# Performance work log

Measured on AMD Instinct MI355X. Metric: run time of the kernel, lower is better.

Reference implementation:

```python
import jax, jax.numpy as jnp
import numpy as np

NEG_SLOPE = 0.2
EPS = 1e-6


def _edge_type_conv(xs, xt, Ws, Wt, a, src, tgt):
    """One hetero edge type: GAT-like edge softmax (unnormalized exp / scatter-sum)."""
    sx = xs @ Ws              # [Ns, d]
    tx = xt @ Wt              # [Nt, d]
    d = sx.shape[1]
    sxg = sx[src]             # [E, d] gather source
    txg = tx[tgt]             # [E, d] gather target
    # concat([sxg, txg]) @ a  ==  sxg @ a[:d] + txg @ a[d:]  (avoids materializing concat)
    score = sxg @ a[:d] + txg @ a[d:]                 # [E, 1]
    att = jnp.exp(jax.nn.leaky_relu(score, NEG_SLOPE))  # [E, 1]
    Nt = xt.shape[0]
    msg = jax.ops.segment_sum(sxg * att, tgt, num_segments=Nt)  # [Nt, d]
    den = jax.ops.segment_sum(att, tgt, num_segments=Nt)        # [Nt, 1]
    return tx + msg / (den + EPS)


def setup_inputs() -> dict:
    key = jax.random.key(0)
    ks = jax.random.split(key, 10)
    N_USER, N_ITEM, D_IN, D_OUT, E = 100000, 100000, 128, 64, 1000000
    glorot_w = np.sqrt(6.0 / (D_IN + D_OUT))
    glorot_a = 1.414 * np.sqrt(6.0 / (2 * D_OUT + 1))
    return {
        "x_user": jax.random.normal(ks[0], (N_USER, D_IN), jnp.float32),
        "x_item": jax.random.normal(ks[1], (N_ITEM, D_IN), jnp.float32),
        "W_ui_src": jax.random.uniform(ks[2], (D_IN, D_OUT), jnp.float32, -glorot_w, glorot_w),
        "W_ui_tgt": jax.random.uniform(ks[3], (D_IN, D_OUT), jnp.float32, -glorot_w, glorot_w),
        "W_iu_src": jax.random.uniform(ks[4], (D_IN, D_OUT), jnp.float32, -glorot_w, glorot_w),
        "W_iu_tgt": jax.random.uniform(ks[5], (D_IN, D_OUT), jnp.float32, -glorot_w, glorot_w),
        "a_ui": jax.random.uniform(ks[6], (2 * D_OUT, 1), jnp.float32, -glorot_a, glorot_a),
        "a_iu": jax.random.uniform(ks[7], (2 * D_OUT, 1), jnp.float32, -glorot_a, glorot_a),
        "edge_ui": jax.random.randint(ks[8], (2, E), 0, N_USER),  # row0: user src, row1: item tgt
        "edge_iu": jax.random.randint(ks[9], (2, E), 0, N_ITEM),  # row0: item src, row1: user tgt
    }


def reference(x_user, x_item, W_ui_src, W_ui_tgt, W_iu_src, W_iu_tgt, a_ui, a_iu, edge_ui, edge_iu):
    # edge type (user, visits, item): target is item
    out_item = _edge_type_conv(x_user, x_item, W_ui_src, W_ui_tgt, a_ui, edge_ui[0], edge_ui[1])
    # edge type (item, visited_by, user): target is user
    out_user = _edge_type_conv(x_item, x_user, W_iu_src, W_iu_tgt, a_iu, edge_iu[0], edge_iu[1])
    return (out_user, out_item)
```

## Files before the change

### kernel.cpp

```cpp
#include <hip/hip_runtime.h>
#include <hip/hip_fp16.h>

#define NEG_SLOPE 0.2f
#define EPS 1e-6f
#define D_IN 128
#define D_OUT 64
#define BN2   192
#define CAP   2304
#define LHIST 2112
#define TILE  8192

__global__ __launch_bounds__(256) void gemm_score_dual(
    const float* __restrict__ x_user, const float* __restrict__ x_item,
    const float* __restrict__ W_ui_src, const float* __restrict__ W_ui_tgt,
    const float* __restrict__ W_iu_src, const float* __restrict__ W_iu_tgt,
    const float* __restrict__ a_ui, const float* __restrict__ a_iu,
    __half* __restrict__ sx_u, __half* __restrict__ sx_i,
    float* __restrict__ out_user, float* __restrict__ out_item,
    float* __restrict__ s_src_ui, float* __restrict__ t_tgt_iu,
    float* __restrict__ s_src_iu, float* __restrict__ t_tgt_ui,
    int nb_u, int N_USER, int N_ITEM)
{
    const bool is_item = (blockIdx.x >= (unsigned)nb_u);
    const float* X  = is_item ? x_item : x_user;
    const float* W1 = is_item ? W_iu_src : W_ui_src;
    const float* W2 = is_item ? W_ui_tgt : W_iu_tgt;
    const float* a1 = is_item ? a_iu : a_ui;
    const float* a2 = is_item ? (a_ui + 64) : (a_iu + 64);
    __half* sfeat   = is_item ? sx_i : sx_u;
    float* tout     = is_item ? out_item : out_user;
    float* s1       = is_item ? s_src_iu : s_src_ui;
    float* s2       = is_item ? t_tgt_ui : t_tgt_iu;
    const int N     = is_item ? N_ITEM : N_USER;
    const int br    = (is_item ? (blockIdx.x - nb_u) : blockIdx.x) * 64;

    __shared__ float Ws[32][128];
    __shared__ float Xs[64][36];
    const int tid = threadIdx.x;
    const int tx = tid & 15;
    const int ty = tid >> 4;

    float acc[4][8];
    #pragma unroll
    for (int r = 0; r < 4; ++r)
        #pragma unroll
        for (int c = 0; c < 8; ++c) acc[r][c] = 0.f;

    for (int kt = 0; kt < D_IN; kt += 32) {
        #pragma unroll
        for (int i = 0; i < 4; ++i) {
            int l = tid + i * 256;
            int row = l >> 5;
            int c4 = (l & 31) << 2;
            const float* wsrc = (c4 < 64) ? &W1[(kt + row) * 64 + c4]
                                          : &W2[(kt + row) * 64 + (c4 - 64)];
            *(float4*)&Ws[row][c4] = *(const float4*)wsrc;
        }
        #pragma unroll
        for (int i = 0; i < 2; ++i) {
            int l = tid + i * 256;
            int row = l >> 3;
            int c4 = (l & 7) << 2;
            float4 v = make_float4(0.f, 0.f, 0.f, 0.f);
            if (br + row < N)
                v = *(const float4*)&X[(size_t)(br + row) * D_IN + kt + c4];
            *(float4*)&Xs[row][c4] = v;
        }
        __syncthreads();
        #pragma unroll 4
        for (int k = 0; k < 32; ++k) {
            float4 wa = *(const float4*)&Ws[k][tx * 4];
            float4 wb = *(const float4*)&Ws[k][64 + tx * 4];
            #pragma unroll
            for (int r = 0; r < 4; ++r) {
                float xv = Xs[ty * 4 + r][k];
                acc[r][0] += xv * wa.x; acc[r][1] += xv * wa.y;
                acc[r][2] += xv * wa.z; acc[r][3] += xv * wa.w;
                acc[r][4] += xv * wb.x; acc[r][5] += xv * wb.y;
                acc[r][6] += xv * wb.z; acc[r][7] += xv * wb.w;
            }
        }
        __syncthreads();
    }

    float a1v[4], a2v[4];
    #pragma unroll
    for (int c = 0; c < 4; ++c) {
        a1v[c] = a1[tx * 4 + c];
        a2v[c] = a2[tx * 4 + c];
    }

    #pragma unroll
    for (int r = 0; r < 4; ++r) {
        int row = br + ty * 4 + r;
        float sv1 = acc[r][0] * a1v[0] + acc[r][1] * a1v[1]
                  + acc[r][2] * a1v[2] + acc[r][3] * a1v[3];
        float sv2 = acc[r][4] * a2v[0] + acc[r][5] * a2v[1]
                  + acc[r][6] * a2v[2] + acc[r][7] * a2v[3];
        sv1 += __shfl_xor(sv1, 1); sv2 += __shfl_xor(sv2, 1);
        sv1 += __shfl_xor(sv1, 2); sv2 += __shfl_xor(sv2, 2);
        sv1 += __shfl_xor(sv1, 4); sv2 += __shfl_xor(sv2, 4);
        sv1 += __shfl_xor(sv1, 8); sv2 += __shfl_xor(sv2, 8);
        if (row < N) {
            union { __half2 h[2]; uint2 u; } pk;
            pk.h[0] = __floats2half2_rn(acc[r][0], acc[r][1]);
            pk.h[1] = __floats2half2_rn(acc[r][2], acc[r][3]);
            *(uint2*)&sfeat[(size_t)row * 64 + tx * 4] = pk.u;
            *(float4*)&tout[(size_t)row * 64 + tx * 4] =
                make_float4(acc[r][4], acc[r][5], acc[r][6], acc[r][7]);
            if (tx == 0) { s1[row] = sv1; s2[row] = sv2; }
        }
    }
}

__global__ __launch_bounds__(512) void bucket_append(
    const int* __restrict__ edge_ui, const int* __restrict__ edge_iu,
    const float* __restrict__ s_src_ui, const float* __restrict__ t_tgt_ui,
    const float* __restrict__ s_src_iu, const float* __restrict__ t_tgt_iu,
    int* __restrict__ cnt, int2* __restrict__ payload,
    int E_a, int E_b, int NB_I, int NB)
{
    __shared__ int lhist[LHIST];
    __shared__ int lbase[LHIST];
    const int tid = threadIdx.x;
    const int ET = E_a + E_b;
    const int tstart = blockIdx.x * TILE;
    int tend = tstart + TILE; if (tend > ET) tend = ET;

    if (NB <= LHIST) {
        for (int i = tid; i < NB; i += 512) lhist[i] = 0;
        __syncthreads();
        for (int e = tstart + tid; e < tend; e += 512) {
            int b;
            if (e < E_a) b = edge_ui[E_a + e] / BN2;
            else         b = NB_I + edge_iu[E_b + (e - E_a)] / BN2;
            atomicAdd(&lhist[b], 1);
        }
        __syncthreads();
        for (int b = tid; b < NB; b += 512) {
            int c = lhist[b];
            lbase[b] = c ? atomicAdd(&cnt[b], c) : 0;
            lhist[b] = 0;
        }
        __syncthreads();
        for (int e = tstart + tid; e < tend; e += 512) {
            int s, t, b; float sc;
            if (e < E_a) {
                s = edge_ui[e]; t = edge_ui[E_a + e];
                sc = s_src_ui[s] + t_tgt_ui[t];
                b = t / BN2;
            } else {
                int eb = e - E_a;
                s = edge_iu[eb]; t = edge_iu[E_b + eb];
                sc = s_src_iu[s] + t_tgt_iu[t];
                b = NB_I + t / BN2;
            }
            sc = (sc > 0.f) ? sc : NEG_SLOPE * sc;
            float att = expf(sc);
            int tl = t % BN2;
            int pos = lbase[b] + atomicAdd(&lhist[b], 1);
            if (pos < CAP)
                payload[(size_t)b * CAP + pos] =
                    make_int2((tl << 20) | s, __float_as_int(att));
        }
    } else {
        for (int e = tstart + tid; e < tend; e += 512) {
            int s, t, b; float sc;
            if (e < E_a) {
                s = edge_ui[e]; t = edge_ui[E_a + e];
                sc = s_src_ui[s] + t_tgt_ui[t];
                b = t / BN2;
            } else {
                int eb = e - E_a;
                s = edge_iu[eb]; t = edge_iu[E_b + eb];
                sc = s_src_iu[s] + t_tgt_iu[t];
                b = NB_I + t / BN2;
            }
            sc = (sc > 0.f) ? sc : NEG_SLOPE * sc;
            float att = expf(sc);
            int tl = t % BN2;
            int pos = atomicAdd(&cnt[b], 1);
            if (pos < CAP)
                payload[(size_t)b * CAP + pos] =
                    make_int2((tl << 20) | s, __float_as_int(att));
        }
    }
}

__global__ __launch_bounds__(512) void bucket_reduce(
    const int* __restrict__ cnt, const int2* __restrict__ payload,
    const __half* __restrict__ sx_u, const __half* __restrict__ sx_i,
    float* __restrict__ out_user, float* __restrict__ out_item,
    int NB_I, int N_USER, int N_ITEM)
{
    __shared__ int2 ord[CAP];
    __shared__ int hist[BN2];
    __shared__ int sc[256];
    __shared__ int ofs[BN2];
    const int b = blockIdx.x;
    const bool item_side = (b < NB_I);
    const __half* sfeat = item_side ? sx_u : sx_i;
    float* outp = item_side ? out_item : out_user;
    const int tbase = (item_side ? b : b - NB_I) * BN2;
    const int Nside = item_side ? N_ITEM : N_USER;
    const int tid = threadIdx.x;

    int n = cnt[b]; if (n > CAP) n = CAP;
    const int2* pl = payload + (size_t)b * CAP;

    for (int i = tid; i < BN2; i += 512) hist[i] = 0;
    __syncthreads();
    for (int i = tid; i < n; i += 512) atomicAdd(&hist[pl[i].x >> 20], 1);
    __syncthreads();
    if (tid < 256) sc[tid] = (tid < BN2) ? hist[tid] : 0;
    __syncthreads();
    #pragma unroll
    for (int d = 1; d < 256; d <<= 1) {
        int v = 0;
        if (tid < 256 && tid >= d) v = sc[tid - d];
        __syncthreads();
        if (tid < 256) sc[tid] += v;
        __syncthreads();
    }
    if (tid < BN2) ofs[tid] = sc[tid] - hist[tid];
    __syncthreads();
    for (int i = tid; i < n; i += 512) {
        int2 p = pl[i];
        int pos = atomicAdd(&ofs[p.x >> 20], 1);
        ord[pos] = p;
    }
    __syncthreads();

    const int wave = tid >> 6, lane = tid & 63;
    for (int tl = wave; tl < BN2; tl += 8) {
        int en = sc[tl];
        int st = en - hist[tl];
        float msg0 = 0.f, msg1 = 0.f, msg2 = 0.f, msg3 = 0.f, den = 0.f;
        int j = st;
        for (; j + 3 < en; j += 4) {
            int2 pA = ord[j];
            int2 pB = ord[j + 1];
            int2 pC = ord[j + 2];
            int2 pD = ord[j + 3];
            float aA = __int_as_float(pA.y);
            float aB = __int_as_float(pB.y);
            float aC = __int_as_float(pC.y);
            float aD = __int_as_float(pD.y);
            float fA = __half2float(sfeat[(size_t)(pA.x & 0xFFFFF) * 64 + lane]);
            float fB = __half2float(sfeat[(size_t)(pB.x & 0xFFFFF) * 64 + lane]);
            float fC = __half2float(sfeat[(size_t)(pC.x & 0xFFFFF) * 64 + lane]);
            float fD = __half2float(sfeat[(size_t)(pD.x & 0xFFFFF) * 64 + lane]);
            msg0 += aA * fA;
            msg1 += aB * fB;
            msg2 += aC * fC;
            msg3 += aD * fD;
            den += (aA + aB) + (aC + aD);
        }
        for (; j < en; ++j) {
            int2 pA = ord[j];
            float aA = __int_as_float(pA.y);
            msg0 += aA * __half2float(sfeat[(size_t)(pA.x & 0xFFFFF) * 64 + lane]);
            den += aA;
        }
        int node = tbase + tl;
        if (node < Nside)
            outp[(size_t)node * 64 + lane] += ((msg0 + msg1) + (msg2 + msg3))
                                              / (den + EPS);
    }
}

extern "C" void kernel_launch(void* const* d_in, const int* in_sizes, int n_in,
                              void* d_out, int out_size, void* d_ws, size_t ws_size,
                              hipStream_t stream) {
    const float* x_user   = (const float*)d_in[0];
    const float* x_item   = (const float*)d_in[1];
    const float* W_ui_src = (const float*)d_in[2];
    const float* W_ui_tgt = (const float*)d_in[3];
    const float* W_iu_src = (const float*)d_in[4];
    const float* W_iu_tgt = (const float*)d_in[5];
    const float* a_ui     = (const float*)d_in[6];
    const float* a_iu     = (const float*)d_in[7];
    const int*   edge_ui  = (const int*)d_in[8];
    const int*   edge_iu  = (const int*)d_in[9];

    const int N_USER = in_sizes[0] / D_IN;
    const int N_ITEM = in_sizes[1] / D_IN;
    const int E_ui = in_sizes[8] / 2;
    const int E_iu = in_sizes[9] / 2;
    const int NMAX = (N_USER > N_ITEM) ? N_USER : N_ITEM;
    const int ET = E_ui + E_iu;
    const int NB_I = (N_ITEM + BN2 - 1) / BN2;
    const int NB_U = (N_USER + BN2 - 1) / BN2;
    const int NB = NB_I + NB_U;

    float* out = (float*)d_out;
    float* out_user = out;
    float* out_item = out + (size_t)N_USER * 64;

    float* w = (float*)d_ws;
    __half* sx_u = (__half*)w;  w += (size_t)NMAX * 32;
    __half* sx_i = (__half*)w;  w += (size_t)NMAX * 32;
    float* s_src_ui = w;  w += N_USER;
    float* t_tgt_iu = w;  w += N_USER;
    float* s_src_iu = w;  w += N_ITEM;
    float* t_tgt_ui = w;  w += N_ITEM;
    int* cnt = (int*)w;   w += (NB + 1) & ~1;
    int2* payload = (int2*)w;  w += (size_t)2 * NB * CAP;

    size_t need_bytes = (size_t)(w - (float*)d_ws) * sizeof(float);
    if (ws_size < need_bytes) return;

    int nb_u = (N_USER + 63) / 64;
    int nb_i = (N_ITEM + 63) / 64;

    gemm_score_dual<<<nb_u + nb_i, 256, 0, stream>>>(
        x_user, x_item, W_ui_src, W_ui_tgt, W_iu_src, W_iu_tgt, a_ui, a_iu,
        sx_u, sx_i, out_user, out_item,
        s_src_ui, t_tgt_iu, s_src_iu, t_tgt_ui,
        nb_u, N_USER, N_ITEM);

    hipMemsetAsync(cnt, 0, (size_t)NB * sizeof(int), stream);
    bucket_append<<<(ET + TILE - 1) / TILE, 512, 0, stream>>>(
        edge_ui, edge_iu, s_src_ui, t_tgt_ui, s_src_iu, t_tgt_iu,
        cnt, payload, E_ui, E_iu, NB_I, NB);

    bucket_reduce<<<NB, 512, 0, stream>>>(
        cnt, payload, sx_u, sx_i, out_user, out_item, NB_I, N_USER, N_ITEM);
}
```

Measured before the change: 385.3 us.

## Replace FP32 SIMT projection GEMM with fp16 MFMA and pre-transposed weights

```diff
diff --git a/kernel.cpp b/kernel.cpp
--- a/kernel.cpp
+++ b/kernel.cpp
@@ -10,10 +10,34 @@
 #define LHIST 2112
 #define TILE  8192
 
-__global__ __launch_bounds__(256) void gemm_score_dual(
-    const float* __restrict__ x_user, const float* __restrict__ x_item,
+typedef __attribute__((ext_vector_type(8))) _Float16 half8;
+typedef __attribute__((ext_vector_type(4))) float  floatx4;
+
+__global__ __launch_bounds__(256) void wt_transpose(
     const float* __restrict__ W_ui_src, const float* __restrict__ W_ui_tgt,
     const float* __restrict__ W_iu_src, const float* __restrict__ W_iu_tgt,
+    __half* __restrict__ wt_u, __half* __restrict__ wt_i)
+{
+    int t = blockIdx.x * 256 + threadIdx.x;
+    if (t >= 8192) return;
+    int kq = t & 31;
+    int c  = (t >> 5) & 127;
+    int side = t >> 12;
+    const float* W1 = side ? W_iu_src : W_ui_src;
+    const float* W2 = side ? W_ui_tgt : W_iu_tgt;
+    __half* wt = side ? wt_i : wt_u;
+    const float* W = (c < 64) ? W1 : W2;
+    int cc = c & 63;
+    __half h[4];
+    #pragma unroll
+    for (int j = 0; j < 4; ++j)
+        h[j] = __float2half(W[(kq * 4 + j) * 64 + cc]);
+    *(uint2*)&wt[(size_t)c * 128 + kq * 4] = *(uint2*)h;
+}
+
+__global__ __launch_bounds__(256) void gemm_mfma_dual(
+    const float* __restrict__ x_user, const float* __restrict__ x_item,
+    const __half* __restrict__ wt_u, const __half* __restrict__ wt_i,
     const float* __restrict__ a_ui, const float* __restrict__ a_iu,
     __half* __restrict__ sx_u, __half* __restrict__ sx_i,
     float* __restrict__ out_user, float* __restrict__ out_item,
@@ -22,94 +46,85 @@
     int nb_u, int N_USER, int N_ITEM)
 {
     const bool is_item = (blockIdx.x >= (unsigned)nb_u);
-    const float* X  = is_item ? x_item : x_user;
-    const float* W1 = is_item ? W_iu_src : W_ui_src;
-    const float* W2 = is_item ? W_ui_tgt : W_iu_tgt;
-    const float* a1 = is_item ? a_iu : a_ui;
-    const float* a2 = is_item ? (a_ui + 64) : (a_iu + 64);
-    __half* sfeat   = is_item ? sx_i : sx_u;
-    float* tout     = is_item ? out_item : out_user;
-    float* s1       = is_item ? s_src_iu : s_src_ui;
-    float* s2       = is_item ? t_tgt_ui : t_tgt_iu;
-    const int N     = is_item ? N_ITEM : N_USER;
-    const int br    = (is_item ? (blockIdx.x - nb_u) : blockIdx.x) * 64;
-
-    __shared__ float Ws[32][128];
-    __shared__ float Xs[64][36];
-    const int tid = threadIdx.x;
-    const int tx = tid & 15;
-    const int ty = tid >> 4;
-
-    float acc[4][8];
-    #pragma unroll
-    for (int r = 0; r < 4; ++r)
+    const float*  X    = is_item ? x_item : x_user;
+    const __half* Wt   = is_item ? wt_i : wt_u;
+    const float*  a1   = is_item ? a_iu : a_ui;
+    const float*  a2   = is_item ? (a_ui + 64) : (a_iu + 64);
+    __half* sfeat      = is_item ? sx_i : sx_u;
+    float*  tout       = is_item ? out_item : out_user;
+    float*  s1         = is_item ? s_src_iu : s_src_ui;
+    float*  s2         = is_item ? t_tgt_ui : t_tgt_iu;
+    const int N        = is_item ? N_ITEM : N_USER;
+    const int br       = (is_item ? (blockIdx.x - nb_u) : blockIdx.x) * 64;
+
+    const int lane = threadIdx.x & 63;
+    const int wv   = threadIdx.x >> 6;
+    const int m15  = lane & 15;
+    const int kg   = lane >> 4;
+    const int xrow = br + wv * 16 + m15;
+    const bool lvalid = (xrow < N);
+
+    floatx4 acc[8];
+    #pragma unroll
+    for (int t = 0; t < 8; ++t)
         #pragma unroll
-        for (int c = 0; c < 8; ++c) acc[r][c] = 0.f;
-
-    for (int kt = 0; kt < D_IN; kt += 32) {
+        for (int r = 0; r < 4; ++r) acc[t][r] = 0.f;
+
+    #pragma unroll
+    for (int kt = 0; kt < 4; ++kt) {
+        half8 afr = {};
+        if (lvalid) {
+            const float* xp = &X[(size_t)xrow * 128 + kt * 32 + kg * 8];
+            float4 x0 = *(const float4*)xp;
+            float4 x1 = *(const float4*)(xp + 4);
+            afr[0] = (_Float16)x0.x; afr[1] = (_Float16)x0.y;
+            afr[2] = (_Float16)x0.z; afr[3] = (_Float16)x0.w;
+            afr[4] = (_Float16)x1.x; afr[5] = (_Float16)x1.y;
+            afr[6] = (_Float16)x1.z; afr[7] = (_Float16)x1.w;
+        }
         #pragma unroll
-        for (int i = 0; i < 4; ++i) {
-            int l = tid + i * 256;
-            int row = l >> 5;
-            int c4 = (l & 31) << 2;
-            const float* wsrc = (c4 < 64) ? &W1[(kt + row) * 64 + c4]
-                                          : &W2[(kt + row) * 64 + (c4 - 64)];
-            *(float4*)&Ws[row][c4] = *(const float4*)wsrc;
-        }
+        for (int tn = 0; tn < 8; ++tn) {
+            half8 bfr = *(const half8*)&Wt[(size_t)(tn * 16 + m15) * 128
+                                           + kt * 32 + kg * 8];
+            acc[tn] = __builtin_amdgcn_mfma_f32_16x16x32_f16(afr, bfr,
+                                                             acc[tn], 0, 0, 0);
+        }
+    }
+
+    float av1[4], av2[4];
+    #pragma unroll
+    for (int tn = 0; tn < 4; ++tn) {
+        av1[tn] = a1[tn * 16 + m15];
+        av2[tn] = a2[tn * 16 + m15];
+    }
+    float sc1[4] = {0.f, 0.f, 0.f, 0.f}, sc2[4] = {0.f, 0.f, 0.f, 0.f};
+    const int srow0 = br + wv * 16 + kg * 4;
+    #pragma unroll
+    for (int tn = 0; tn < 8; ++tn) {
         #pragma unroll
-        for (int i = 0; i < 2; ++i) {
-            int l = tid + i * 256;
-            int row = l >> 3;
-            int c4 = (l & 7) << 2;
-            float4 v = make_float4(0.f, 0.f, 0.f, 0.f);
-            if (br + row < N)
-                v = *(const float4*)&X[(size_t)(br + row) * D_IN + kt + c4];
-            *(float4*)&Xs[row][c4] = v;
-        }
-        __syncthreads();
-        #pragma unroll 4
-        for (int k = 0; k < 32; ++k) {
-            float4 wa = *(const float4*)&Ws[k][tx * 4];
-            float4 wb = *(const float4*)&Ws[k][64 + tx * 4];
-            #pragma unroll
-            for (int r = 0; r < 4; ++r) {
-                float xv = Xs[ty * 4 + r][k];
-                acc[r][0] += xv * wa.x; acc[r][1] += xv * wa.y;
-                acc[r][2] += xv * wa.z; acc[r][3] += xv * wa.w;
-                acc[r][4] += xv * wb.x; acc[r][5] += xv * wb.y;
-                acc[r][6] += xv * wb.z; acc[r][7] += xv * wb.w;
+        for (int r = 0; r < 4; ++r) {
+            float v = acc[tn][r];
+            int srow = srow0 + r;
+            if (tn < 4) {
+                sc1[r] += v * av1[tn];
+                if (srow < N)
+                    sfeat[(size_t)srow * 64 + tn * 16 + m15] = __float2half(v);
+            } else {
+                sc2[r] += v * av2[tn - 4];
+                if (srow < N)
+                    tout[(size_t)srow * 64 + (tn - 4) * 16 + m15] = v;
             }
         }
-        __syncthreads();
-    }
-
-    float a1v[4], a2v[4];
-    #pragma unroll
-    for (int c = 0; c < 4; ++c) {
-        a1v[c] = a1[tx * 4 + c];
-        a2v[c] = a2[tx * 4 + c];
-    }
-
+    }
     #pragma unroll
     for (int r = 0; r < 4; ++r) {
-        int row = br + ty * 4 + r;
-        float sv1 = acc[r][0] * a1v[0] + acc[r][1] * a1v[1]
-                  + acc[r][2] * a1v[2] + acc[r][3] * a1v[3];
-        float sv2 = acc[r][4] * a2v[0] + acc[r][5] * a2v[1]
-                  + acc[r][6] * a2v[2] + acc[r][7] * a2v[3];
-        sv1 += __shfl_xor(sv1, 1); sv2 += __shfl_xor(sv2, 1);
-        sv1 += __shfl_xor(sv1, 2); sv2 += __shfl_xor(sv2, 2);
-        sv1 += __shfl_xor(sv1, 4); sv2 += __shfl_xor(sv2, 4);
-        sv1 += __shfl_xor(sv1, 8); sv2 += __shfl_xor(sv2, 8);
-        if (row < N) {
-            union { __half2 h[2]; uint2 u; } pk;
-            pk.h[0] = __floats2half2_rn(acc[r][0], acc[r][1]);
-            pk.h[1] = __floats2half2_rn(acc[r][2], acc[r][3]);
-            *(uint2*)&sfeat[(size_t)row * 64 + tx * 4] = pk.u;
-            *(float4*)&tout[(size_t)row * 64 + tx * 4] =
-                make_float4(acc[r][4], acc[r][5], acc[r][6], acc[r][7]);
-            if (tx == 0) { s1[row] = sv1; s2[row] = sv2; }
-        }
+        float v1 = sc1[r], v2 = sc2[r];
+        v1 += __shfl_xor(v1, 1); v2 += __shfl_xor(v2, 1);
+        v1 += __shfl_xor(v1, 2); v2 += __shfl_xor(v2, 2);
+        v1 += __shfl_xor(v1, 4); v2 += __shfl_xor(v2, 4);
+        v1 += __shfl_xor(v1, 8); v2 += __shfl_xor(v2, 8);
+        int srow = srow0 + r;
+        if (m15 == 0 && srow < N) { s1[srow] = v1; s2[srow] = v2; }
     }
 }
 
@@ -298,6 +313,8 @@
     float* out_item = out + (size_t)N_USER * 64;
 
     float* w = (float*)d_ws;
+    __half* wt_u = (__half*)w;  w += 128 * 64;
+    __half* wt_i = (__half*)w;  w += 128 * 64;
     __half* sx_u = (__half*)w;  w += (size_t)NMAX * 32;
     __half* sx_i = (__half*)w;  w += (size_t)NMAX * 32;
     float* s_src_ui = w;  w += N_USER;
@@ -313,8 +330,11 @@
     int nb_u = (N_USER + 63) / 64;
     int nb_i = (N_ITEM + 63) / 64;
 
-    gemm_score_dual<<<nb_u + nb_i, 256, 0, stream>>>(
-        x_user, x_item, W_ui_src, W_ui_tgt, W_iu_src, W_iu_tgt, a_ui, a_iu,
+    wt_transpose<<<32, 256, 0, stream>>>(
+        W_ui_src, W_ui_tgt, W_iu_src, W_iu_tgt, wt_u, wt_i);
+
+    gemm_mfma_dual<<<nb_u + nb_i, 256, 0, stream>>>(
+        x_user, x_item, wt_u, wt_i, a_ui, a_iu,
         sx_u, sx_i, out_user, out_item,
         s_src_ui, t_tgt_iu, s_src_iu, t_tgt_ui,
         nb_u, N_USER, N_ITEM);
```

New measurement: 373.6 us. -3.0%, faster.
